# Performance work log

Hardware: AMD Instinct MI355X
Metric: run time of the kernel (lower is better)

## Reference

```python
import jax, jax.numpy as jnp
import numpy as np

EPS = 1e-12  # torch F.normalize eps

def setup_inputs() -> dict:
    key = jax.random.key(0)
    ks = jax.random.split(key, 3)
    B, N, C, H, K = 4, 4096, 512, 8, 64
    x = jax.random.normal(ks[0], (B, N, C), dtype=jnp.float32)
    W_qkvv = jax.random.normal(ks[1], (4 * C, C), dtype=jnp.float32) * (1.0 / np.sqrt(C))
    # init_: uniform(-1/sqrt(K), 1/sqrt(K)) over [N, K]
    std = 1.0 / np.sqrt(K)
    EF = jax.random.uniform(ks[2], (N, K), dtype=jnp.float32, minval=-std, maxval=std)
    temperature = jnp.ones((H, 1, 1), dtype=jnp.float32)
    temperature2 = jnp.ones((H, 1, 1), dtype=jnp.float32)
    return {"x": x, "W_qkvv": W_qkvv, "EF": EF,
            "temperature": temperature, "temperature2": temperature2}

def _l2norm(t):
    # torch.nn.functional.normalize(dim=-1): x / max(||x||_2, eps)
    n = jnp.sqrt(jnp.sum(t * t, axis=-1, keepdims=True))
    return t / jnp.maximum(n, EPS)

def reference(x, W_qkvv, EF, temperature, temperature2):
    B, N, C = x.shape
    H = temperature.shape[0]
    d = C // H
    # fused QKVV projection (no bias)
    qkvv = (x @ W_qkvv.T).reshape(B, N, 4, H, d)
    qkvv = jnp.transpose(qkvv, (2, 0, 3, 1, 4))  # [4,B,H,N,d]
    # transpose last two dims -> [B,H,d,N]
    q = jnp.swapaxes(qkvv[0], -2, -1)
    k = jnp.swapaxes(qkvv[1], -2, -1)
    v_CA = jnp.swapaxes(qkvv[2], -2, -1)
    v_SA = jnp.swapaxes(qkvv[3], -2, -1)
    # Linformer-style EF projection over token axis: [B,H,d,N] x [N,K] -> [B,H,d,K]
    k_proj = jnp.einsum('bhdn,nk->bhdk', k, EF)
    v_proj = jnp.einsum('bhdn,nk->bhdk', v_SA, EF)
    # L2-normalize q,k over token axis
    qn = _l2norm(q)
    kn = _l2norm(k)
    # channel attention: [B,H,d,d]
    attn_CA = jax.nn.softmax(jnp.einsum('bhdn,bhen->bhde', qn, kn) * temperature, axis=-1)
    x_CA = jnp.einsum('bhde,bhen->bhdn', attn_CA, v_CA)           # [B,H,d,N]
    x_CA = jnp.transpose(x_CA, (0, 3, 1, 2)).reshape(B, N, C)      # [B,N,C]
    # spatial attention via projected K: [B,H,N,K]
    attn_SA = jax.nn.softmax(jnp.einsum('bhdn,bhdk->bhnk', qn, k_proj) * temperature2, axis=-1)
    x_SA = jnp.einsum('bhnk,bhdk->bhnd', attn_SA, v_proj)          # [B,H,N,d]
    # faithful to the original: permute(0,3,1,2) then reshape(B,N,C)
    x_SA = jnp.transpose(x_SA, (0, 3, 1, 2)).reshape(B, N, C)
    return x_CA + x_SA
```

## Files before the change

kernel.cpp:

```cpp
#include <hip/hip_runtime.h>

typedef unsigned short u16;
typedef unsigned int u32;
typedef __attribute__((ext_vector_type(8))) short s16x8;
typedef __attribute__((ext_vector_type(4))) float f32x4;

#define MFMA16(a,b,c) __builtin_amdgcn_mfma_f32_16x16x32_bf16(a,b,c,0,0,0)

__device__ __forceinline__ u16 f2bf(float f){
  u32 u = __builtin_bit_cast(u32, f);
  return (u16)((u + 0x7FFFu + ((u >> 16) & 1u)) >> 16);
}
__device__ __forceinline__ float b2f(u16 s){
  u32 u = ((u32)s) << 16;
  return __builtin_bit_cast(float, u);
}
__device__ __forceinline__ void async16(const void* g, void* l){
  __builtin_amdgcn_global_load_lds((const __attribute__((address_space(1))) u32*)g,
                                   (__attribute__((address_space(3))) u32*)l, 16, 0, 0);
}


__global__ __launch_bounds__(256) void k_convert(const float4* __restrict__ x4,
                                                 const float4* __restrict__ w4,
                                                 const float* __restrict__ EF,
                                                 u16* __restrict__ Xb, u16* __restrict__ Wb,
                                                 u16* __restrict__ EFt){
  int i = blockIdx.x * 256 + threadIdx.x;
  if (i < 2097152){
    float4 v = x4[i];
    u32 lo = (u32)f2bf(v.x) | ((u32)f2bf(v.y) << 16);
    u32 hi = (u32)f2bf(v.z) | ((u32)f2bf(v.w) << 16);
    *(uint2*)(&Xb[(size_t)i*4]) = make_uint2(lo, hi);
  } else if (i < 2097152 + 262144){
    int j = i - 2097152;
    float4 v = w4[j];
    u32 lo = (u32)f2bf(v.x) | ((u32)f2bf(v.y) << 16);
    u32 hi = (u32)f2bf(v.z) | ((u32)f2bf(v.w) << 16);
    *(uint2*)(&Wb[(size_t)j*4]) = make_uint2(lo, hi);
  } else if (i < 2097152 + 262144 + 262144){
    int j = i - 2097152 - 262144;
    int kk = j >> 12, nn = j & 4095;
    EFt[(size_t)kk*4096 + nn] = f2bf(EF[(size_t)nn*64 + kk]);
  }
}

__global__ __launch_bounds__(512, 2) void k_gemm(const u16* __restrict__ Wb,
                                                 const u16* __restrict__ Xb,
                                                 u16* __restrict__ Out){
  __shared__ u16 As[2][2][128*64];
  __shared__ u16 Bs[2][2][128*64];
  int bid = blockIdx.x;
  int sbid = (bid & 7) * 64 + (bid >> 3);
  int ot = sbid >> 6, mt = sbid & 63;
  int o0 = ot * 256, m0 = mt * 256;
  int t = threadIdx.x;
  int lane = t & 63, wid = t >> 6;
  int wr = wid >> 2, wc = wid & 3;
  int l15 = lane & 15, l4 = lane >> 4;

#define STAGE_TILE(kt_, db_)                                                    \
  {                                                                             \
    int kb_ = (kt_) * 64;                                                       \
    int srow_ = t >> 3, sg_ = (t & 7) ^ (srow_ & 7);                            \
    _Pragma("unroll")                                                           \
    for (int hf = 0; hf < 2; ++hf){                                             \
      _Pragma("unroll")                                                         \
      for (int c = 0; c < 2; ++c){                                              \
        int row = c*64 + srow_;                                                 \
        async16(Wb + (size_t)(o0 + hf*128 + row) * 512 + kb_ + sg_*8,           \
                &As[db_][hf][row*64 + (t & 7)*8]);                              \
        async16(Xb + (size_t)(m0 + hf*128 + row) * 512 + kb_ + sg_*8,           \
                &Bs[db_][hf][row*64 + (t & 7)*8]);                              \
      }                                                                         \
    }                                                                           \
  }

  f32x4 acc[8][4];
#pragma unroll
  for (int a = 0; a < 8; ++a)
#pragma unroll
    for (int b = 0; b < 4; ++b) acc[a][b] = (f32x4){0.f, 0.f, 0.f, 0.f};

  STAGE_TILE(0, 0);
  asm volatile("s_waitcnt vmcnt(0)" ::: "memory");
  __builtin_amdgcn_s_barrier();
  asm volatile("" ::: "memory");

  s16x8 bfr[4];
  for (int kt = 0; kt < 8; ++kt){
    int db = kt & 1;
    const u16* Abase = &As[db][wr][0];
    const u16* Bbase = &Bs[db][wc >> 1][0];
#pragma unroll
    for (int p = 0; p < 4; ++p){
      const int ks = p >> 1, rfh = p & 1;
      s16x8 af[4];
#pragma unroll
      for (int i = 0; i < 4; ++i){
        int row = (rfh*4 + i)*16 + l15;
        af[i] = *(const s16x8*)(Abase + row*64 + ((ks*4 + l4) ^ (row & 7))*8);
      }
      if (rfh == 0){
#pragma unroll
        for (int cf = 0; cf < 4; ++cf){
          int row = (wc & 1)*64 + cf*16 + l15;
          bfr[cf] = *(const s16x8*)(Bbase + row*64 + ((ks*4 + l4) ^ (row & 7))*8);
        }
      }
      if (p == 0 && kt < 7) STAGE_TILE(kt + 1, db ^ 1);
      __builtin_amdgcn_s_barrier();
      asm volatile("" ::: "memory");
      __builtin_amdgcn_s_setprio(1);
#pragma unroll
      for (int i = 0; i < 4; ++i)
#pragma unroll
        for (int cf = 0; cf < 4; ++cf)
          acc[rfh*4 + i][cf] = MFMA16(af[i], bfr[cf], acc[rfh*4 + i][cf]);
      __builtin_amdgcn_s_setprio(0);
      if (p == 3 && kt < 7) asm volatile("s_waitcnt vmcnt(0)" ::: "memory");
      __builtin_amdgcn_s_barrier();
      asm volatile("" ::: "memory");
    }
  }
#undef STAGE_TILE

#pragma unroll
  for (int rf = 0; rf < 8; ++rf)
#pragma unroll
    for (int cf = 0; cf < 4; ++cf){
      int o = o0 + wr*128 + rf*16 + l4*4;
      int m = m0 + wc*64 + cf*16 + l15;
#pragma unroll
      for (int r = 0; r < 4; ++r) Out[(size_t)(o + r) * 16384 + m] = f2bf(acc[rf][cf][r]);
    }
}

__global__ __launch_bounds__(256) void k_rnorm(const u16* __restrict__ QK,
                                               float* __restrict__ rq, float* __restrict__ rk){
  int job = blockIdx.x * 4 + (threadIdx.x >> 6);
  int o = job >> 2, b = job & 3;
  int lane = threadIdx.x & 63;
  const u16* row = QK + (size_t)o * 16384 + (size_t)b * 4096;
  float s = 0.f;
#pragma unroll
  for (int it = 0; it < 8; ++it){
    s16x8 v = *(const s16x8*)(&row[it * 512 + lane * 8]);
#pragma unroll
    for (int j = 0; j < 8; ++j){ float f = b2f((u16)v[j]); s += f * f; }
  }
  for (int off = 32; off; off >>= 1) s += __shfl_down(s, off);
  if (lane == 0){
    float r = 1.f / fmaxf(sqrtf(s), 1e-12f);
    if (o < 512) rq[b * 512 + o] = r;
    else         rk[b * 512 + (o - 512)] = r;
  }
}

__global__ __launch_bounds__(256) void k_acc1(const u16* __restrict__ QK,
                                              const u16* __restrict__ EFt,
                                              float* __restrict__ Pp){
  __shared__ u16 Ab[2][64*128];
  __shared__ u16 Bb[2][64*128];
  int bid = blockIdx.x;
  int p = bid >> 8;
  int rem = bid & 255;
  int bh = rem >> 3, s = rem & 7;
  int b = bh >> 3, h = bh & 7;
  int t = threadIdx.x, lane = t & 63, w = t >> 6, l15 = lane & 15, l4 = lane >> 4;
  int abase = (p == 0 ? 0 : (p == 1 ? 512 : 1536)) + h * 64;
  const u16* Aglob = QK + (size_t)abase * 16384 + (size_t)b * 4096 + s * 512;
  const u16* Bglob;
  size_t bstride;
  if (p == 0){ Bglob = QK + (size_t)(512 + h*64) * 16384 + (size_t)b * 4096 + s * 512; bstride = 16384; }
  else       { Bglob = EFt + s * 512; bstride = 4096; }
  int srow = t >> 4, sslot = t & 15;

#define STAGE_ACC(ch, buf)                                                        \
  {                                                                               \
    int n0_ = (ch) * 128;                                                         \
    _Pragma("unroll")                                                             \
    for (int c = 0; c < 4; ++c){                                                  \
      int row = c*16 + srow;                                                      \
      int sg = sslot ^ (row & 7);                                                 \
      async16(Aglob + (size_t)row * 16384 + n0_ + sg*8, &Ab[buf][row*128 + sslot*8]); \
    }                                                                             \
    _Pragma("unroll")                                                             \
    for (int c = 0; c < 4; ++c){                                                  \
      int row = c*16 + srow;                                                      \
      int sg = sslot ^ (row & 7);                                                 \
      async16(Bglob + (size_t)row * bstride + n0_ + sg*8, &Bb[buf][row*128 + sslot*8]); \
    }                                                                             \
  }

  f32x4 acc[4];
#pragma unroll
  for (int c = 0; c < 4; ++c) acc[c] = (f32x4){0.f,0.f,0.f,0.f};

  STAGE_ACC(0, 0);
#pragma unroll
  for (int ch = 0; ch < 4; ++ch){
    int buf = ch & 1;
    if (ch < 3){
      STAGE_ACC(ch + 1, buf ^ 1);
      asm volatile("s_waitcnt vmcnt(8)" ::: "memory");
    } else {
      asm volatile("s_waitcnt vmcnt(0)" ::: "memory");
    }
    __builtin_amdgcn_s_barrier();
    asm volatile("" ::: "memory");
    int arow = w*16 + l15;
#pragma unroll
    for (int ks = 0; ks < 4; ++ks){
      s16x8 a = *(const s16x8*)(&Ab[buf][arow*128 + (((ks*4 + l4) ^ (arow & 7)))*8]);
#pragma unroll
      for (int cf = 0; cf < 4; ++cf){
        int brow = cf*16 + l15;
        s16x8 bb = *(const s16x8*)(&Bb[buf][brow*128 + (((ks*4 + l4) ^ (brow & 7)))*8]);
        acc[cf] = MFMA16(a, bb, acc[cf]);
      }
    }
    __builtin_amdgcn_s_barrier();
    asm volatile("" ::: "memory");
  }

  float* out = Pp + ((size_t)(bh * 3 + p) * 8 + s) * 4096;
#pragma unroll
  for (int cf = 0; cf < 4; ++cf)
#pragma unroll
    for (int r = 0; r < 4; ++r){
      int rr = w*16 + l4*4 + r;
      int cc = cf*16 + l15;
      int off = (p == 1) ? (cc * 64 + rr) : (rr * 64 + cc);
      out[off] = acc[cf][r];
    }
#undef STAGE_ACC
}

__global__ __launch_bounds__(256) void k_fin(const float* __restrict__ Pp,
                                             const float* __restrict__ rq,
                                             const float* __restrict__ rk,
                                             const float* __restrict__ t1,
                                             const float* __restrict__ t2,
                                             u16* __restrict__ Pca,
                                             u16* __restrict__ kpb,
                                             u16* __restrict__ vpb){
  int bh = blockIdx.x;
  int b = bh >> 3, h = bh & 7;
  int t = threadIdx.x;
  int row = t >> 2, q4 = t & 3;
  const float* base = Pp + (size_t)bh * 3 * 8 * 4096;
  float t1h = t1[h], t2h = t2[h];
  const float* rqh = rq + b*512 + h*64;
  const float* rkh = rk + b*512 + h*64;
  int sA = (((q4*2)     ^ (row & 7)) << 3);
  int sB = (((q4*2 + 1) ^ (row & 7)) << 3);

  {
    float v[16];
#pragma unroll
    for (int i = 0; i < 4; ++i){
      f32x4 a = (f32x4){0.f,0.f,0.f,0.f};
#pragma unroll
      for (int s = 0; s < 8; ++s)
        a += *(const f32x4*)(base + (size_t)s * 4096 + t*16 + i*4);
#pragma unroll
      for (int j = 0; j < 4; ++j) v[i*4 + j] = a[j];
    }
    float sq = rqh[row] * t1h;
#pragma unroll
    for (int e = 0; e < 16; ++e) v[e] *= sq * rkh[q4*16 + e];
    float mx = v[0];
#pragma unroll
    for (int e = 1; e < 16; ++e) mx = fmaxf(mx, v[e]);
    mx = fmaxf(mx, __shfl_xor(mx, 1));
    mx = fmaxf(mx, __shfl_xor(mx, 2));
    float sum = 0.f;
#pragma unroll
    for (int e = 0; e < 16; ++e){ v[e] = __expf(v[e] - mx); sum += v[e]; }
    sum += __shfl_xor(sum, 1);
    sum += __shfl_xor(sum, 2);
    float inv = 1.f / sum;
    s16x8 o0, o1;
#pragma unroll
    for (int e = 0; e < 8; ++e){ o0[e] = (short)f2bf(v[e] * inv); o1[e] = (short)f2bf(v[8+e] * inv); }
    *(s16x8*)(&Pca[(size_t)bh*4096 + row*64 + sA]) = o0;
    *(s16x8*)(&Pca[(size_t)bh*4096 + row*64 + sB]) = o1;
  }
  {
    const float* p1 = base + 8 * 4096;
    float v[16];
#pragma unroll
    for (int i = 0; i < 4; ++i){
      f32x4 a = (f32x4){0.f,0.f,0.f,0.f};
#pragma unroll
      for (int s = 0; s < 8; ++s)
        a += *(const f32x4*)(p1 + (size_t)s * 4096 + t*16 + i*4);
#pragma unroll
      for (int j = 0; j < 4; ++j) v[i*4 + j] = a[j];
    }
    s16x8 o0, o1;
#pragma unroll
    for (int e = 0; e < 8; ++e){
      o0[e] = (short)f2bf(v[e]   * rqh[q4*16 + e]     * t2h);
      o1[e] = (short)f2bf(v[8+e] * rqh[q4*16 + 8 + e] * t2h);
    }
    *(s16x8*)(&kpb[(size_t)bh*4096 + row*64 + sA]) = o0;
    *(s16x8*)(&kpb[(size_t)bh*4096 + row*64 + sB]) = o1;
  }
  {
    const float* p2 = base + 16 * 4096;
    float v[16];
#pragma unroll
    for (int i = 0; i < 4; ++i){
      f32x4 a = (f32x4){0.f,0.f,0.f,0.f};
#pragma unroll
      for (int s = 0; s < 8; ++s)
        a += *(const f32x4*)(p2 + (size_t)s * 4096 + t*16 + i*4);
#pragma unroll
      for (int j = 0; j < 4; ++j) v[i*4 + j] = a[j];
    }
    s16x8 o0, o1;
#pragma unroll
    for (int e = 0; e < 8; ++e){ o0[e] = (short)f2bf(v[e]); o1[e] = (short)f2bf(v[8+e]); }
    *(s16x8*)(&vpb[(size_t)bh*4096 + row*64 + sA]) = o0;
    *(s16x8*)(&vpb[(size_t)bh*4096 + row*64 + sB]) = o1;
  }
}

__global__ __launch_bounds__(256) void k_ca_pv(const u16* __restrict__ QK,
                                               const u16* __restrict__ Pca,
                                               float* __restrict__ out){
  __shared__ u16 Pl[64*64];
  __shared__ u16 Vt[64*64];
  __shared__ float Sx[64*64];
  int bid = blockIdx.x;
  int ch = bid & 63, bh = bid >> 6, b = bh >> 3, h = bh & 7;
  int n0 = ch * 64;
  int t = threadIdx.x, lane = t & 63, w = t >> 6, l15 = lane & 15, l4 = lane >> 4;
  {
    const u16* src = Pca + (size_t)bh * 4096;
#pragma unroll
    for (int c = 0; c < 2; ++c)
      async16(src + (c*256 + t)*8, &Pl[(c*256 + t)*8]);
  }
  const u16* Vg = QK + (size_t)(1024 + h*64) * 16384 + (size_t)b*4096 + n0;
#pragma unroll
  for (int pass = 0; pass < 2; ++pass){
    int idx = pass*256 + t;
    int e = idx >> 3, j0 = (idx & 7) * 8, g = idx & 7;
    s16x8 v = *(const s16x8*)(Vg + (size_t)e * 16384 + j0);
#pragma unroll
    for (int i = 0; i < 8; ++i){
      int jj = (i + e + g) & 7;
      int j = j0 + jj;
      Vt[j*64 + ((((e>>3) ^ jj)) << 3) + (e & 7)] = (u16)v[jj];
    }
  }
  __syncthreads();
  f32x4 acc[4];
#pragma unroll
  for (int c = 0; c < 4; ++c) acc[c] = (f32x4){0.f,0.f,0.f,0.f};
  int ar = w*16 + l15;
#pragma unroll
  for (int ks = 0; ks < 2; ++ks){
    s16x8 a = *(const s16x8*)(&Pl[ar*64 + (((ks*4 + l4) ^ (ar & 7)))*8]);
#pragma unroll
    for (int cf = 0; cf < 4; ++cf){
      int br = cf*16 + l15;
      s16x8 bb = *(const s16x8*)(&Vt[br*64 + (((ks*4 + l4) ^ (br & 7)))*8]);
      acc[cf] = MFMA16(a, bb, acc[cf]);
    }
  }
#pragma unroll
  for (int cf = 0; cf < 4; ++cf)
#pragma unroll
    for (int r = 0; r < 4; ++r){
      int d = w*16 + l4*4 + r, j = cf*16 + l15;
      Sx[j*64 + d] = acc[cf][r];
    }
  __syncthreads();
#pragma unroll
  for (int i = 0; i < 4; ++i){
    int idx = t + 256 * i;
    int j = idx >> 4, v = idx & 15;
    float4 val;
    val.x = Sx[j*64 + v*4 + 0]; val.y = Sx[j*64 + v*4 + 1];
    val.z = Sx[j*64 + v*4 + 2]; val.w = Sx[j*64 + v*4 + 3];
    *(float4*)(&out[((size_t)(b*4096 + n0 + j)) * 512 + h*64 + v*4]) = val;
  }
}

__global__ __launch_bounds__(256) void k_sa(const u16* __restrict__ QK,
                                            const u16* __restrict__ kpb,
                                            const u16* __restrict__ vpb,
                                            float* __restrict__ out){
  __shared__ u16 Qt[64*64];
  __shared__ u16 kpl[64*64];
  __shared__ u16 vpl[64*64];
  __shared__ float Sf[64*64];
  int bid = blockIdx.x;
  int ch = bid & 63, bh = bid >> 6, b = bh >> 3, h = bh & 7;
  int n0 = ch * 64;
  int t = threadIdx.x, lane = t & 63, w = t >> 6, l15 = lane & 15, l4 = lane >> 4;
#pragma unroll
  for (int c = 0; c < 2; ++c){
    async16(kpb + (size_t)bh*4096 + (c*256 + t)*8, &kpl[(c*256 + t)*8]);
    async16(vpb + (size_t)bh*4096 + (c*256 + t)*8, &vpl[(c*256 + t)*8]);
  }
  const u16* Qg = QK + (size_t)(h*64) * 16384 + (size_t)b*4096 + n0;
#pragma unroll
  for (int pass = 0; pass < 2; ++pass){
    int idx = pass*256 + t;
    int dd = idx >> 3, j0 = (idx & 7) * 8, g = idx & 7;
    s16x8 v = *(const s16x8*)(Qg + (size_t)dd * 16384 + j0);
#pragma unroll
    for (int i = 0; i < 8; ++i){
      int jj = (i + dd + g) & 7;
      int j = j0 + jj;
      Qt[j*64 + ((((dd>>3) ^ jj)) << 3) + (dd & 7)] = (u16)v[jj];
    }
  }
  __syncthreads();
  f32x4 acc[4];
#pragma unroll
  for (int c = 0; c < 4; ++c) acc[c] = (f32x4){0.f,0.f,0.f,0.f};
  int ar = w*16 + l15;
#pragma unroll
  for (int ks = 0; ks < 2; ++ks){
    s16x8 a = *(const s16x8*)(&Qt[ar*64 + (((ks*4 + l4) ^ (ar & 7)))*8]);
#pragma unroll
    for (int cf = 0; cf < 4; ++cf){
      int br = cf*16 + l15;
      s16x8 bb = *(const s16x8*)(&kpl[br*64 + (((ks*4 + l4) ^ (br & 7)))*8]);
      acc[cf] = MFMA16(a, bb, acc[cf]);
    }
  }
#pragma unroll
  for (int r = 0; r < 4; ++r){
    float mx = fmaxf(fmaxf(acc[0][r], acc[1][r]), fmaxf(acc[2][r], acc[3][r]));
    mx = fmaxf(mx, __shfl_xor(mx, 1));
    mx = fmaxf(mx, __shfl_xor(mx, 2));
    mx = fmaxf(mx, __shfl_xor(mx, 4));
    mx = fmaxf(mx, __shfl_xor(mx, 8));
    float sum = 0.f;
#pragma unroll
    for (int cf = 0; cf < 4; ++cf){ acc[cf][r] = __expf(acc[cf][r] - mx); sum += acc[cf][r]; }
    sum += __shfl_xor(sum, 1);
    sum += __shfl_xor(sum, 2);
    sum += __shfl_xor(sum, 4);
    sum += __shfl_xor(sum, 8);
    float inv = 1.f / sum;
#pragma unroll
    for (int cf = 0; cf < 4; ++cf) acc[cf][r] *= inv;
  }
#pragma unroll
  for (int cf = 0; cf < 4; ++cf)
#pragma unroll
    for (int r = 0; r < 4; ++r){
      int j = w*16 + l4*4 + r;
      int kslot = cf*2 + (l15 >> 3);
      Qt[j*64 + ((kslot ^ (j & 7)) << 3) + (l15 & 7)] = f2bf(acc[cf][r]);
    }
  __syncthreads();
  f32x4 acc2[4];
#pragma unroll
  for (int c = 0; c < 4; ++c) acc2[c] = (f32x4){0.f,0.f,0.f,0.f};
#pragma unroll
  for (int ks = 0; ks < 2; ++ks){
    s16x8 a = *(const s16x8*)(&Qt[ar*64 + (((ks*4 + l4) ^ (ar & 7)))*8]);
#pragma unroll
    for (int cf = 0; cf < 4; ++cf){
      int br = cf*16 + l15;
      s16x8 bb = *(const s16x8*)(&vpl[br*64 + (((ks*4 + l4) ^ (br & 7)))*8]);
      acc2[cf] = MFMA16(a, bb, acc2[cf]);
    }
  }
#pragma unroll
  for (int cf = 0; cf < 4; ++cf)
#pragma unroll
    for (int r = 0; r < 4; ++r){
      int j = w*16 + l4*4 + r, dd = cf*16 + l15;
      Sf[dd*64 + j] = acc2[cf][r];
    }
  __syncthreads();
#pragma unroll
  for (int i = 0; i < 4; ++i){
    int idx = t + 256 * i;
    int dd = idx >> 4, v = idx & 15;
    size_t p = (size_t)b*2097152 + (size_t)dd*32768 + (size_t)h*4096 + n0 + v*4;
    float4 cur = *(float4*)(&out[p]);
    cur.x += Sf[dd*64 + v*4 + 0]; cur.y += Sf[dd*64 + v*4 + 1];
    cur.z += Sf[dd*64 + v*4 + 2]; cur.w += Sf[dd*64 + v*4 + 3];
    *(float4*)(&out[p]) = cur;
  }
}

extern "C" void kernel_launch(void* const* d_in, const int* in_sizes, int n_in,
                              void* d_out, int out_size, void* d_ws, size_t ws_size,
                              hipStream_t stream) {
  const float* x  = (const float*)d_in[0];
  const float* Wq = (const float*)d_in[1];
  const float* EF = (const float*)d_in[2];
  const float* t1 = (const float*)d_in[3];
  const float* t2 = (const float*)d_in[4];
  float* out = (float*)d_out;

  u16* Xb  = (u16*)d_ws;
  u16* Wb  = Xb + 8388608;
  u16* EFt = Wb + 1048576;
  u16* QK  = EFt + 262144;
  float* rq  = (float*)(QK + 33554432);
  float* rk  = rq + 2048;
  u16* kpb = (u16*)(rk + 2048);
  u16* vpb = kpb + 131072;
  u16* Pca = vpb + 131072;
  float* Pp = (float*)d_ws;

  k_convert<<<10240, 256, 0, stream>>>((const float4*)x, (const float4*)Wq, EF, Xb, Wb, EFt);
  k_gemm   <<<512,  512, 0, stream>>>(Wb, Xb, QK);
  k_rnorm  <<<1024, 256, 0, stream>>>(QK, rq, rk);
  k_acc1   <<<768,  256, 0, stream>>>(QK, EFt, Pp);
  k_fin    <<<32,   256, 0, stream>>>(Pp, rq, rk, t1, t2, Pca, kpb, vpb);
  k_ca_pv  <<<2048, 256, 0, stream>>>(QK, Pca, out);
  k_sa     <<<2048, 256, 0, stream>>>(QK, kpb, vpb, out);
}
```

Before: 198.7 us.

## Spread k_fin over 128 blocks and remap GEMM block swizzle

```diff
diff --git a/kernel.cpp b/kernel.cpp
--- a/kernel.cpp
+++ b/kernel.cpp
@@ -51,8 +51,8 @@
   __shared__ u16 As[2][2][128*64];
   __shared__ u16 Bs[2][2][128*64];
   int bid = blockIdx.x;
-  int sbid = (bid & 7) * 64 + (bid >> 3);
-  int ot = sbid >> 6, mt = sbid & 63;
+  int x = bid & 7, c = bid >> 3;
+  int ot = c >> 3, mt = x * 8 + (c & 7);
   int o0 = ot * 256, m0 = mt * 256;
   int t = threadIdx.x;
   int lane = t & 63, wid = t >> 6;
@@ -66,8 +66,8 @@
     _Pragma("unroll")                                                           \
     for (int hf = 0; hf < 2; ++hf){                                             \
       _Pragma("unroll")                                                         \
-      for (int c = 0; c < 2; ++c){                                              \
-        int row = c*64 + srow_;                                                 \
+      for (int cc = 0; cc < 2; ++cc){                                           \
+        int row = cc*64 + srow_;                                                \
         async16(Wb + (size_t)(o0 + hf*128 + row) * 512 + kb_ + sg_*8,           \
                 &As[db_][hf][row*64 + (t & 7)*8]);                              \
         async16(Xb + (size_t)(m0 + hf*128 + row) * 512 + kb_ + sg_*8,           \
@@ -245,86 +245,63 @@
                                              u16* __restrict__ Pca,
                                              u16* __restrict__ kpb,
                                              u16* __restrict__ vpb){
-  int bh = blockIdx.x;
+  int bid = blockIdx.x;
+  int bh = bid >> 2, rg = bid & 3;
   int b = bh >> 3, h = bh & 7;
   int t = threadIdx.x;
-  int row = t >> 2, q4 = t & 3;
-  const float* base = Pp + (size_t)bh * 3 * 8 * 4096;
+  int lr = t >> 4, c4 = t & 15;
+  int row = rg * 16 + lr;
+  const float* base = Pp + (size_t)bh * 3 * 8 * 4096 + row*64 + c4*4;
   float t1h = t1[h], t2h = t2[h];
   const float* rqh = rq + b*512 + h*64;
   const float* rkh = rk + b*512 + h*64;
-  int sA = (((q4*2)     ^ (row & 7)) << 3);
-  int sB = (((q4*2 + 1) ^ (row & 7)) << 3);
+  int so = row*64 + (((c4 >> 1) ^ (row & 7)) << 3) + ((c4 & 1) << 2);
 
   {
-    float v[16];
-#pragma unroll
-    for (int i = 0; i < 4; ++i){
-      f32x4 a = (f32x4){0.f,0.f,0.f,0.f};
-#pragma unroll
-      for (int s = 0; s < 8; ++s)
-        a += *(const f32x4*)(base + (size_t)s * 4096 + t*16 + i*4);
-#pragma unroll
-      for (int j = 0; j < 4; ++j) v[i*4 + j] = a[j];
-    }
+    f32x4 a = (f32x4){0.f,0.f,0.f,0.f};
+#pragma unroll
+    for (int s = 0; s < 8; ++s) a += *(const f32x4*)(base + (size_t)s * 4096);
     float sq = rqh[row] * t1h;
-#pragma unroll
-    for (int e = 0; e < 16; ++e) v[e] *= sq * rkh[q4*16 + e];
-    float mx = v[0];
-#pragma unroll
-    for (int e = 1; e < 16; ++e) mx = fmaxf(mx, v[e]);
+    float v[4];
+#pragma unroll
+    for (int j = 0; j < 4; ++j) v[j] = a[j] * sq * rkh[c4*4 + j];
+    float mx = fmaxf(fmaxf(v[0], v[1]), fmaxf(v[2], v[3]));
     mx = fmaxf(mx, __shfl_xor(mx, 1));
     mx = fmaxf(mx, __shfl_xor(mx, 2));
+    mx = fmaxf(mx, __shfl_xor(mx, 4));
+    mx = fmaxf(mx, __shfl_xor(mx, 8));
     float sum = 0.f;
 #pragma unroll
-    for (int e = 0; e < 16; ++e){ v[e] = __expf(v[e] - mx); sum += v[e]; }
+    for (int j = 0; j < 4; ++j){ v[j] = __expf(v[j] - mx); sum += v[j]; }
     sum += __shfl_xor(sum, 1);
     sum += __shfl_xor(sum, 2);
+    sum += __shfl_xor(sum, 4);
+    sum += __shfl_xor(sum, 8);
     float inv = 1.f / sum;
-    s16x8 o0, o1;
-#pragma unroll
-    for (int e = 0; e < 8; ++e){ o0[e] = (short)f2bf(v[e] * inv); o1[e] = (short)f2bf(v[8+e] * inv); }
-    *(s16x8*)(&Pca[(size_t)bh*4096 + row*64 + sA]) = o0;
-    *(s16x8*)(&Pca[(size_t)bh*4096 + row*64 + sB]) = o1;
+    u32 lo = (u32)f2bf(v[0]*inv) | ((u32)f2bf(v[1]*inv) << 16);
+    u32 hi = (u32)f2bf(v[2]*inv) | ((u32)f2bf(v[3]*inv) << 16);
+    *(uint2*)(&Pca[(size_t)bh*4096 + so]) = make_uint2(lo, hi);
   }
   {
     const float* p1 = base + 8 * 4096;
-    float v[16];
-#pragma unroll
-    for (int i = 0; i < 4; ++i){
-      f32x4 a = (f32x4){0.f,0.f,0.f,0.f};
-#pragma unroll
-      for (int s = 0; s < 8; ++s)
-        a += *(const f32x4*)(p1 + (size_t)s * 4096 + t*16 + i*4);
-#pragma unroll
-      for (int j = 0; j < 4; ++j) v[i*4 + j] = a[j];
-    }
-    s16x8 o0, o1;
-#pragma unroll
-    for (int e = 0; e < 8; ++e){
-      o0[e] = (short)f2bf(v[e]   * rqh[q4*16 + e]     * t2h);
-      o1[e] = (short)f2bf(v[8+e] * rqh[q4*16 + 8 + e] * t2h);
-    }
-    *(s16x8*)(&kpb[(size_t)bh*4096 + row*64 + sA]) = o0;
-    *(s16x8*)(&kpb[(size_t)bh*4096 + row*64 + sB]) = o1;
+    f32x4 a = (f32x4){0.f,0.f,0.f,0.f};
+#pragma unroll
+    for (int s = 0; s < 8; ++s) a += *(const f32x4*)(p1 + (size_t)s * 4096);
+    float v[4];
+#pragma unroll
+    for (int j = 0; j < 4; ++j) v[j] = a[j] * rqh[c4*4 + j] * t2h;
+    u32 lo = (u32)f2bf(v[0]) | ((u32)f2bf(v[1]) << 16);
+    u32 hi = (u32)f2bf(v[2]) | ((u32)f2bf(v[3]) << 16);
+    *(uint2*)(&kpb[(size_t)bh*4096 + so]) = make_uint2(lo, hi);
   }
   {
     const float* p2 = base + 16 * 4096;
-    float v[16];
-#pragma unroll
-    for (int i = 0; i < 4; ++i){
-      f32x4 a = (f32x4){0.f,0.f,0.f,0.f};
-#pragma unroll
-      for (int s = 0; s < 8; ++s)
-        a += *(const f32x4*)(p2 + (size_t)s * 4096 + t*16 + i*4);
-#pragma unroll
-      for (int j = 0; j < 4; ++j) v[i*4 + j] = a[j];
-    }
-    s16x8 o0, o1;
-#pragma unroll
-    for (int e = 0; e < 8; ++e){ o0[e] = (short)f2bf(v[e]); o1[e] = (short)f2bf(v[8+e]); }
-    *(s16x8*)(&vpb[(size_t)bh*4096 + row*64 + sA]) = o0;
-    *(s16x8*)(&vpb[(size_t)bh*4096 + row*64 + sB]) = o1;
+    f32x4 a = (f32x4){0.f,0.f,0.f,0.f};
+#pragma unroll
+    for (int s = 0; s < 8; ++s) a += *(const f32x4*)(p2 + (size_t)s * 4096);
+    u32 lo = (u32)f2bf(a[0]) | ((u32)f2bf(a[1]) << 16);
+    u32 hi = (u32)f2bf(a[2]) | ((u32)f2bf(a[3]) << 16);
+    *(uint2*)(&vpb[(size_t)bh*4096 + so]) = make_uint2(lo, hi);
   }
 }
 
@@ -521,7 +498,7 @@
   k_gemm   <<<512,  512, 0, stream>>>(Wb, Xb, QK);
   k_rnorm  <<<1024, 256, 0, stream>>>(QK, rq, rk);
   k_acc1   <<<768,  256, 0, stream>>>(QK, EFt, Pp);
-  k_fin    <<<32,   256, 0, stream>>>(Pp, rq, rk, t1, t2, Pca, kpb, vpb);
+  k_fin    <<<128,  256, 0, stream>>>(Pp, rq, rk, t1, t2, Pca, kpb, vpb);
   k_ca_pv  <<<2048, 256, 0, stream>>>(QK, Pca, out);
   k_sa     <<<2048, 256, 0, stream>>>(QK, kpb, vpb, out);
 }
```

New measurement: 191.3 us. -3.7%, faster.
